# Optimization experiments

Measured on AMD Instinct MI355X. Metric: run time of the kernel, lower is better.

Reference implementation:

```python
import jax, jax.numpy as jnp
import numpy as np

CUTOFF = 8.0
N_NODES = 100000
N_EDGES = 3200000
HIDDEN = 256
VOCAB = 178


def _swish(x):
    return x * jax.nn.sigmoid(x)


def _safe_norm(v):
    # L2 norm over last axis with torch-style zero subgradient at 0
    ss = jnp.sum(v * v, axis=-1)
    return jnp.where(ss == 0, 0.0, jnp.sqrt(jnp.where(ss == 0, 1.0, ss)))


def _safe_atan2(b, a):
    # atan2 with finite grad at (0,0); forward value identical (atan2(0,0)=0)
    deg = (a == 0) & (b == 0)
    return jnp.arctan2(b, jnp.where(deg, 1.0, a))


def _scatter_argmin(d, idx, num_seg):
    # replicates torch_scatter.scatter_min argmin output (empty segments -> 0)
    E = d.shape[0]
    mn = jax.ops.segment_min(d, idx, num_segments=num_seg)
    cand = jnp.where(d == mn[idx], jnp.arange(E), E)
    am = jax.ops.segment_min(cand, idx, num_segments=num_seg)
    return jnp.where(am >= E, 0, am)


def _dist_calc(cutoff, vecs, dist, i, j, num_nodes):
    argmin0 = _scatter_argmin(dist, i, num_nodes)
    n0 = j[argmin0]
    dist1 = dist + jnp.zeros_like(dist).at[argmin0].set(cutoff)
    argmin1 = _scatter_argmin(dist1, i, num_nodes)
    n1 = j[argmin1]
    argmin0_j = _scatter_argmin(dist, j, num_nodes)
    n0_j = i[argmin0_j]
    dist1_j = dist + jnp.zeros_like(dist).at[argmin0_j].set(cutoff)
    argmin1_j = _scatter_argmin(dist1_j, j, num_nodes)
    n1_j = i[argmin1_j]

    n0 = n0[i]
    n1 = n1[i]
    n0_j = n0_j[j]
    n1_j = n1_j[j]

    idx_iref = jnp.where(n0 == j, argmin1[i], argmin0[i])
    idx_jref = jnp.where(n0_j == i, argmin1_j[j], argmin0_j[j])

    pos_ji = vecs                      # [E,3]
    pos_in0 = vecs[argmin0[i]]         # vecs[argmin0][i]
    pos_in1 = vecs[argmin1[i]]
    pos_iref = vecs[idx_iref]
    pos_jref_j = vecs[idx_jref]

    a = jnp.sum(-pos_ji * pos_in0, axis=-1)
    b = _safe_norm(jnp.cross(-pos_ji, pos_in0))
    theta = _safe_atan2(b, a)
    theta = jnp.where(theta < 0, theta + jnp.pi, theta)

    dist_ji = _safe_norm(pos_ji)

    plane1 = jnp.cross(-pos_ji, pos_in0)
    plane2 = jnp.cross(-pos_ji, pos_in1)
    a = jnp.sum(plane1 * plane2, axis=-1)
    b = jnp.sum(jnp.cross(plane1, plane2) * pos_ji, axis=-1) / dist_ji
    phi = _safe_atan2(b, a)
    phi = jnp.where(phi < 0, phi + jnp.pi, phi)

    plane1 = jnp.cross(pos_ji, pos_jref_j)
    plane2 = jnp.cross(pos_ji, pos_iref)
    a = jnp.sum(plane1 * plane2, axis=-1)
    b = jnp.sum(jnp.cross(plane1, plane2) * pos_ji, axis=-1) / dist_ji
    tau = _safe_atan2(b, a)
    tau = jnp.where(tau < 0, tau + jnp.pi, tau)

    return dist, theta, phi, tau


def setup_inputs() -> dict:
    key = jax.random.key(0)
    k1, k2, k3, k4, k5 = jax.random.split(key, 5)
    x = jax.random.randint(k1, (N_NODES,), 0, VOCAB)
    pos = jax.random.normal(k2, (N_NODES, 3), jnp.float32) * 3.0
    i = jax.random.randint(k3, (N_EDGES,), 0, N_NODES)
    off = jax.random.randint(k4, (N_EDGES,), 1, N_NODES)
    j = (i + off) % N_NODES  # no self-edges -> dist > 0
    edge_index = jnp.stack([i, j])
    emb_weight = jax.random.normal(k5, (VOCAB, HIDDEN), jnp.float32)
    return {"x": x, "pos": pos, "edge_index": edge_index, "emb_weight": emb_weight}


def reference(x, pos, edge_index, emb_weight):
    i, j = edge_index[0], edge_index[1]
    vecs = pos[j] - pos[i]          # [E,3]
    dist = _safe_norm(vecs)         # [E]
    h = _swish(emb_weight[x])       # [N,H]
    dist, theta, phi, tau = _dist_calc(CUTOFF, vecs, dist, i, j, pos.shape[0])
    return h, dist, theta, phi, tau
```

## Files before the change

kernel.cpp:

```cpp
#include <hip/hip_runtime.h>
#include <math.h>

#define HID 256
#define PI_F 3.14159265358979323846f
typedef unsigned long long ull;

struct F3 { float x, y, z; };

__device__ __forceinline__ F3 crossc(F3 a, F3 b) {
    F3 r;
    float t1 = a.z * b.y;
    r.x = __builtin_fmaf(a.y, b.z, -t1);
    float t2 = a.x * b.z;
    r.y = __builtin_fmaf(a.z, b.x, -t2);
    float t3 = a.y * b.x;
    r.z = __builtin_fmaf(a.x, b.y, -t3);
    return r;
}
__device__ __forceinline__ float dotf(F3 a, F3 b) {
#pragma clang fp contract(off)
    float px = a.x * b.x;
    float py = a.y * b.y;
    float pz = a.z * b.z;
    return (px + py) + pz;
}
__device__ __forceinline__ float sqrt_cr(float ss) {
    return (float)sqrt((double)ss);
}
__device__ __forceinline__ float safe_atan2(float b, float a) {
    float aa = (a == 0.f && b == 0.f) ? 1.f : a;
    return atan2f(b, aa);
}
__device__ __forceinline__ F3 loadp(const float* __restrict__ pos, int n) {
    F3 r;
    r.x = pos[3 * n + 0];
    r.y = pos[3 * n + 1];
    r.z = pos[3 * n + 2];
    return r;
}
__device__ __forceinline__ F3 subv(F3 a, F3 b) {
#pragma clang fp contract(off)
    F3 r;
    r.x = a.x - b.x;
    r.y = a.y - b.y;
    r.z = a.z - b.z;
    return r;
}
__device__ __forceinline__ ull umin64(ull a, ull b) { return a < b ? a : b; }

__device__ __forceinline__ unsigned xcc_id() {
    return __builtin_amdgcn_s_getreg((3u << 11) | 20u) & 7u;
}

__device__ __forceinline__ void insert2_loc(ull* __restrict__ s, unsigned db, ull key) {
    unsigned hi2 = ((const unsigned*)s)[3];
    if (db > hi2) return;
    unsigned hi1 = ((const unsigned*)s)[1];
    if (db <= hi1) {
        ull ret = __hip_atomic_fetch_min(&s[0], key, __ATOMIC_RELAXED,
                                         __HIP_MEMORY_SCOPE_WORKGROUP);
        ull loser = ret > key ? ret : key;
        if (loser != ~0ull)
            __hip_atomic_fetch_min(&s[1], loser, __ATOMIC_RELAXED,
                                   __HIP_MEMORY_SCOPE_WORKGROUP);
    } else {
        __hip_atomic_fetch_min(&s[1], key, __ATOMIC_RELAXED,
                               __HIP_MEMORY_SCOPE_WORKGROUP);
    }
}

__device__ __forceinline__ void merge8(const ull* __restrict__ slots8, size_t twoN,
                                       int n, ull& m1, ull& m2) {
    m1 = ~0ull; m2 = ~0ull;
#pragma unroll
    for (int c = 0; c < 8; c++) {
        ull a = slots8[(size_t)c * twoN + 2 * (size_t)n];
        ull b = slots8[(size_t)c * twoN + 2 * (size_t)n + 1];
        if (a < m1) { m2 = m1; m1 = a; } else if (a < m2) m2 = a;
        if (b < m1) { m2 = m1; m1 = b; } else if (b < m2) m2 = b;
    }
}

__global__ void k_pass1(const int* __restrict__ ei, const int* __restrict__ ej,
                        const float* __restrict__ pos, float* __restrict__ dist,
                        ull* __restrict__ slots8A, ull* __restrict__ slots8B,
                        const unsigned* __restrict__ thrA, const unsigned* __restrict__ thrB,
                        size_t twoN, int e0, int e1) {
#pragma clang fp contract(off)
    int e = e0 + blockIdx.x * blockDim.x + threadIdx.x;
    if (e >= e1) return;
    unsigned c = xcc_id();
    ull* sA = slots8A + (size_t)c * twoN;
    ull* sB = slots8B + (size_t)c * twoN;
    int ii = ei[e], jj = ej[e];
    F3 v = subv(loadp(pos, jj), loadp(pos, ii));
    float sx = v.x * v.x;
    float sy = v.y * v.y;
    float sz = v.z * v.z;
    float ss = (sx + sy) + sz;
    float d = (ss == 0.f) ? 0.f : sqrt_cr(ss);
    dist[e] = d;
    unsigned db = __float_as_uint(d);
    ull key = ((ull)db << 32) | (unsigned)e;
    if (db <= thrA[ii]) insert2_loc(&sA[2 * (size_t)ii], db, key);
    if (db <= thrB[jj]) insert2_loc(&sB[2 * (size_t)jj], db, key);
}

__global__ void k_snapshot(const ull* __restrict__ slots8A, const ull* __restrict__ slots8B,
                           unsigned* __restrict__ thrA, unsigned* __restrict__ thrB,
                           size_t twoN, int N) {
    int n = blockIdx.x * blockDim.x + threadIdx.x;
    if (n >= N) return;
    ull m1, m2;
    merge8(slots8A, twoN, n, m1, m2);
    thrA[n] = (unsigned)(m2 >> 32);
    merge8(slots8B, twoN, n, m1, m2);
    thrB[n] = (unsigned)(m2 >> 32);
}

__global__ void k_prep(const ull* __restrict__ slots8A, const ull* __restrict__ slots8B,
                       const int* __restrict__ ei, const int* __restrict__ ej,
                       const float* __restrict__ pos,
                       float4* __restrict__ nodeI, float4* __restrict__ nodeJ,
                       int* __restrict__ a0i, int* __restrict__ a0j,
                       unsigned* __restrict__ flags, size_t twoN, int N) {
#pragma clang fp contract(off)
    int n = blockIdx.x * blockDim.x + threadIdx.x;
    if (n >= N) return;

    ull k1, k2;
    merge8(slots8A, twoN, n, k1, k2);
    int a0, a1;
    if (k1 == ~0ull) {
        a0 = 0; a1 = 0;
        atomicOr(&flags[0], 1u);
    } else {
        a0 = (int)(k1 & 0xffffffffu);
        float d0 = __uint_as_float((unsigned)(k1 >> 32));
        ull mkey = ((ull)__float_as_uint(d0 + 8.0f) << 32) | (unsigned)a0;
        if (k2 == ~0ull) a1 = a0;
        else a1 = (mkey < k2) ? a0 : (int)(k2 & 0xffffffffu);
    }
    a0i[n] = a0;
    F3 in0 = subv(loadp(pos, ej[a0]), loadp(pos, ei[a0]));
    int n0 = ej[a0];
    F3 in1 = subv(loadp(pos, ej[a1]), loadp(pos, ei[a1]));
    nodeI[2 * (size_t)n]     = make_float4(in0.x, in0.y, in0.z, __int_as_float(n0));
    nodeI[2 * (size_t)n + 1] = make_float4(in1.x, in1.y, in1.z, 0.f);

    ull q1, q2;
    merge8(slots8B, twoN, n, q1, q2);
    int b0, b1;
    if (q1 == ~0ull) {
        b0 = 0; b1 = 0;
        atomicOr(&flags[1], 1u);
    } else {
        b0 = (int)(q1 & 0xffffffffu);
        float d0 = __uint_as_float((unsigned)(q1 >> 32));
        ull mkey = ((ull)__float_as_uint(d0 + 8.0f) << 32) | (unsigned)b0;
        if (q2 == ~0ull) b1 = b0;
        else b1 = (mkey < q2) ? b0 : (int)(q2 & 0xffffffffu);
    }
    a0j[n] = b0;
    F3 w0 = subv(loadp(pos, ej[b0]), loadp(pos, ei[b0]));
    int m0 = ei[b0];
    F3 w1 = subv(loadp(pos, ej[b1]), loadp(pos, ei[b1]));
    nodeJ[2 * (size_t)n]     = make_float4(w0.x, w0.y, w0.z, __int_as_float(m0));
    nodeJ[2 * (size_t)n + 1] = make_float4(w1.x, w1.y, w1.z, 0.f);
}

__global__ void k_fix(const unsigned* __restrict__ flags,
                      const int* __restrict__ ei, const int* __restrict__ ej,
                      const float* __restrict__ dist,
                      const int* __restrict__ a0i, const int* __restrict__ a0j,
                      const float* __restrict__ pos,
                      float4* __restrict__ nodeI, float4* __restrict__ nodeJ, int E) {
#pragma clang fp contract(off)
    __shared__ ull smin[256];
    int side = blockIdx.x;
    if (flags[side] == 0u) return;
    const int* seg = (side == 0) ? ei : ej;
    int s = seg[0];
    int marked = (side == 0) ? a0i[s] : a0j[s];
    ull local = ~0ull;
    for (int e = threadIdx.x; e < E; e += 256) {
        if (seg[e] != s) continue;
        float d = dist[e];
        float dm = (e == marked || e == 0) ? (d + 8.0f) : d;
        ull key = ((ull)__float_as_uint(dm) << 32) | (unsigned)e;
        local = umin64(local, key);
    }
    smin[threadIdx.x] = local;
    __syncthreads();
    for (int w = 128; w > 0; w >>= 1) {
        if (threadIdx.x < w) smin[threadIdx.x] = umin64(smin[threadIdx.x], smin[threadIdx.x + w]);
        __syncthreads();
    }
    if (threadIdx.x == 0) {
        int a1 = (smin[0] == ~0ull) ? 0 : (int)(smin[0] & 0xffffffffu);
        F3 v = subv(loadp(pos, ej[a1]), loadp(pos, ei[a1]));
        if (side == 0) nodeI[2 * (size_t)s + 1] = make_float4(v.x, v.y, v.z, 0.f);
        else           nodeJ[2 * (size_t)s + 1] = make_float4(v.x, v.y, v.z, 0.f);
    }
}

__global__ void k_angles(const int* __restrict__ ei, const int* __restrict__ ej,
                         const float* __restrict__ pos, const float* __restrict__ dist,
                         const float4* __restrict__ nodeI, const float4* __restrict__ nodeJ,
                         float* __restrict__ theta, float* __restrict__ phi,
                         float* __restrict__ tau, int E) {
    int e = blockIdx.x * blockDim.x + threadIdx.x;
    if (e >= E) return;
    int ii = ei[e], jj = ej[e];

    float4 A0 = nodeI[2 * (size_t)ii];
    float4 A1 = nodeI[2 * (size_t)ii + 1];
    float4 B0 = nodeJ[2 * (size_t)jj];
    float4 B1 = nodeJ[2 * (size_t)jj + 1];
    int n0 = __float_as_int(A0.w);
    int m0 = __float_as_int(B0.w);

    F3 in0; in0.x = A0.x; in0.y = A0.y; in0.z = A0.z;
    F3 in1; in1.x = A1.x; in1.y = A1.y; in1.z = A1.z;
    F3 w0;  w0.x = B0.x;  w0.y = B0.y;  w0.z = B0.z;
    F3 w1;  w1.x = B1.x;  w1.y = B1.y;  w1.z = B1.z;

    F3 iref = (n0 == jj) ? in1 : in0;
    F3 jref = (m0 == ii) ? w1 : w0;

    F3 p = subv(loadp(pos, jj), loadp(pos, ii));
    F3 mp;
    mp.x = -p.x; mp.y = -p.y; mp.z = -p.z;

    float a = dotf(mp, in0);
    F3 c1 = crossc(mp, in0);
    float ssb = dotf(c1, c1);
    float b = (ssb == 0.f) ? 0.f : sqrt_cr(ssb);
    float th = safe_atan2(b, a);
    if (th < 0.f) th += PI_F;

    float dji = dist[e];

    F3 pl2 = crossc(mp, in1);
    a = dotf(c1, pl2);
    F3 cc = crossc(c1, pl2);
    b = dotf(cc, p) / dji;
    float ph = safe_atan2(b, a);
    if (ph < 0.f) ph += PI_F;

    F3 t1 = crossc(p, jref);
    F3 t2 = crossc(p, iref);
    a = dotf(t1, t2);
    cc = crossc(t1, t2);
    b = dotf(cc, p) / dji;
    float ta = safe_atan2(b, a);
    if (ta < 0.f) ta += PI_F;

    theta[e] = th;
    phi[e] = ph;
    tau[e] = ta;
}

__global__ void k_embed(const int* __restrict__ x, const float* __restrict__ w,
                        float* __restrict__ h, int total4) {
    int t = blockIdx.x * blockDim.x + threadIdx.x;
    if (t >= total4) return;
    int n = t >> 6;
    int c = t & 63;
    int row = x[n];
    float4 v = *reinterpret_cast<const float4*>(w + (size_t)row * HID + c * 4);
    float4 o;
    o.x = v.x / (1.f + expf(-v.x));
    o.y = v.y / (1.f + expf(-v.y));
    o.z = v.z / (1.f + expf(-v.z));
    o.w = v.w / (1.f + expf(-v.w));
    *reinterpret_cast<float4*>(h + (size_t)n * HID + c * 4) = o;
}

extern "C" void kernel_launch(void* const* d_in, const int* in_sizes, int n_in,
                              void* d_out, int out_size, void* d_ws, size_t ws_size,
                              hipStream_t stream) {
    const int* x = (const int*)d_in[0];
    const float* pos = (const float*)d_in[1];
    const int* eidx = (const int*)d_in[2];
    const float* emb = (const float*)d_in[3];

    const int N = in_sizes[0];
    const int E = in_sizes[2] / 2;
    const int* ei = eidx;
    const int* ej = eidx + E;

    float* out = (float*)d_out;
    float* out_h = out;
    float* out_dist = out + (size_t)N * HID;
    float* out_theta = out_dist + E;
    float* out_phi = out_theta + E;
    float* out_tau = out_phi + E;

    size_t twoN = 2 * (size_t)N;
    ull* slots8A = (ull*)out_h;
    ull* slots8B = slots8A + 8 * twoN;
    unsigned* thrA = (unsigned*)(slots8B + 8 * twoN);
    unsigned* thrB = thrA + N;
    float4* nodeI = (float4*)(thrB + N);
    float4* nodeJ = nodeI + twoN;
    int* a0i = (int*)(nodeJ + twoN);
    int* a0j = a0i + N;
    unsigned* flags = (unsigned*)(a0j + N);

    const int BS = 256;
    int gN = (N + BS - 1) / BS;
    int total4 = N * (HID / 4);
    int gH = (total4 + BS - 1) / BS;

    hipMemsetAsync(slots8A, 0xFF, 16 * twoN * sizeof(ull) + 2 * (size_t)N * sizeof(unsigned), stream);
    hipMemsetAsync(flags, 0, 2 * sizeof(unsigned), stream);

    int bounds[5] = {0, E / 8, E / 4, E / 2, E};
    for (int k = 0; k < 4; k++) {
        int lo = bounds[k], hi = bounds[k + 1];
        if (hi <= lo) continue;
        int g = (hi - lo + BS - 1) / BS;
        k_pass1<<<g, BS, 0, stream>>>(ei, ej, pos, out_dist, slots8A, slots8B,
                                      thrA, thrB, twoN, lo, hi);
        if (k < 3)
            k_snapshot<<<gN, BS, 0, stream>>>(slots8A, slots8B, thrA, thrB, twoN, N);
    }

    k_prep<<<gN, BS, 0, stream>>>(slots8A, slots8B, ei, ej, pos,
                                  nodeI, nodeJ, a0i, a0j, flags, twoN, N);
    k_fix<<<2, BS, 0, stream>>>(flags, ei, ej, out_dist, a0i, a0j, pos,
                                nodeI, nodeJ, E);
    k_angles<<<(E + BS - 1) / BS, BS, 0, stream>>>(ei, ej, pos, out_dist, nodeI, nodeJ,
                                                   out_theta, out_phi, out_tau, E);
    k_embed<<<gH, BS, 0, stream>>>(x, emb, out_h, total4);
}
```

Before: 389.7 us.

## Drop threshold-filtered chunked pass1 and cache edge vectors for angle kernel

Replaces the four-chunk pass1 with per-node threshold snapshots by a single pass over all edges that always attempts the top-2 atomic insert. It also stores each edge's vector in a scratch buffer so the angle kernel reads 12 contiguous bytes instead of gathering two random positions. This removes three snapshot kernels and several launches. In exchange every edge now issues atomics, where before most were filtered out by the thresholds, and an extra 12-byte-per-edge write and read is added.

```diff
diff --git a/kernel.cpp b/kernel.cpp
--- a/kernel.cpp
+++ b/kernel.cpp
@@ -83,17 +83,20 @@
 
 __global__ void k_pass1(const int* __restrict__ ei, const int* __restrict__ ej,
                         const float* __restrict__ pos, float* __restrict__ dist,
+                        float* __restrict__ vecs,
                         ull* __restrict__ slots8A, ull* __restrict__ slots8B,
-                        const unsigned* __restrict__ thrA, const unsigned* __restrict__ thrB,
-                        size_t twoN, int e0, int e1) {
-#pragma clang fp contract(off)
-    int e = e0 + blockIdx.x * blockDim.x + threadIdx.x;
-    if (e >= e1) return;
+                        size_t twoN, int E) {
+#pragma clang fp contract(off)
+    int e = blockIdx.x * blockDim.x + threadIdx.x;
+    if (e >= E) return;
     unsigned c = xcc_id();
     ull* sA = slots8A + (size_t)c * twoN;
     ull* sB = slots8B + (size_t)c * twoN;
     int ii = ei[e], jj = ej[e];
     F3 v = subv(loadp(pos, jj), loadp(pos, ii));
+    vecs[3 * (size_t)e + 0] = v.x;
+    vecs[3 * (size_t)e + 1] = v.y;
+    vecs[3 * (size_t)e + 2] = v.z;
     float sx = v.x * v.x;
     float sy = v.y * v.y;
     float sz = v.z * v.z;
@@ -102,20 +105,8 @@
     dist[e] = d;
     unsigned db = __float_as_uint(d);
     ull key = ((ull)db << 32) | (unsigned)e;
-    if (db <= thrA[ii]) insert2_loc(&sA[2 * (size_t)ii], db, key);
-    if (db <= thrB[jj]) insert2_loc(&sB[2 * (size_t)jj], db, key);
-}
-
-__global__ void k_snapshot(const ull* __restrict__ slots8A, const ull* __restrict__ slots8B,
-                           unsigned* __restrict__ thrA, unsigned* __restrict__ thrB,
-                           size_t twoN, int N) {
-    int n = blockIdx.x * blockDim.x + threadIdx.x;
-    if (n >= N) return;
-    ull m1, m2;
-    merge8(slots8A, twoN, n, m1, m2);
-    thrA[n] = (unsigned)(m2 >> 32);
-    merge8(slots8B, twoN, n, m1, m2);
-    thrB[n] = (unsigned)(m2 >> 32);
+    insert2_loc(&sA[2 * (size_t)ii], db, key);
+    insert2_loc(&sB[2 * (size_t)jj], db, key);
 }
 
 __global__ void k_prep(const ull* __restrict__ slots8A, const ull* __restrict__ slots8B,
@@ -205,7 +196,7 @@
 }
 
 __global__ void k_angles(const int* __restrict__ ei, const int* __restrict__ ej,
-                         const float* __restrict__ pos, const float* __restrict__ dist,
+                         const float* __restrict__ vecs, const float* __restrict__ dist,
                          const float4* __restrict__ nodeI, const float4* __restrict__ nodeJ,
                          float* __restrict__ theta, float* __restrict__ phi,
                          float* __restrict__ tau, int E) {
@@ -228,7 +219,10 @@
     F3 iref = (n0 == jj) ? in1 : in0;
     F3 jref = (m0 == ii) ? w1 : w0;
 
-    F3 p = subv(loadp(pos, jj), loadp(pos, ii));
+    F3 p;
+    p.x = vecs[3 * (size_t)e + 0];
+    p.y = vecs[3 * (size_t)e + 1];
+    p.z = vecs[3 * (size_t)e + 2];
     F3 mp;
     mp.x = -p.x; mp.y = -p.y; mp.z = -p.z;
 
@@ -300,38 +294,29 @@
     size_t twoN = 2 * (size_t)N;
     ull* slots8A = (ull*)out_h;
     ull* slots8B = slots8A + 8 * twoN;
-    unsigned* thrA = (unsigned*)(slots8B + 8 * twoN);
-    unsigned* thrB = thrA + N;
-    float4* nodeI = (float4*)(thrB + N);
+    float4* nodeI = (float4*)(slots8B + 8 * twoN);
     float4* nodeJ = nodeI + twoN;
-    int* a0i = (int*)(nodeJ + twoN);
+    float* vecs = (float*)(nodeJ + twoN);
+    int* a0i = (int*)(vecs + 3 * (size_t)E);
     int* a0j = a0i + N;
     unsigned* flags = (unsigned*)(a0j + N);
 
     const int BS = 256;
+    int gE = (E + BS - 1) / BS;
     int gN = (N + BS - 1) / BS;
     int total4 = N * (HID / 4);
     int gH = (total4 + BS - 1) / BS;
 
-    hipMemsetAsync(slots8A, 0xFF, 16 * twoN * sizeof(ull) + 2 * (size_t)N * sizeof(unsigned), stream);
+    hipMemsetAsync(slots8A, 0xFF, 16 * twoN * sizeof(ull), stream);
     hipMemsetAsync(flags, 0, 2 * sizeof(unsigned), stream);
 
-    int bounds[5] = {0, E / 8, E / 4, E / 2, E};
-    for (int k = 0; k < 4; k++) {
-        int lo = bounds[k], hi = bounds[k + 1];
-        if (hi <= lo) continue;
-        int g = (hi - lo + BS - 1) / BS;
-        k_pass1<<<g, BS, 0, stream>>>(ei, ej, pos, out_dist, slots8A, slots8B,
-                                      thrA, thrB, twoN, lo, hi);
-        if (k < 3)
-            k_snapshot<<<gN, BS, 0, stream>>>(slots8A, slots8B, thrA, thrB, twoN, N);
-    }
-
+    k_pass1<<<gE, BS, 0, stream>>>(ei, ej, pos, out_dist, vecs,
+                                   slots8A, slots8B, twoN, E);
     k_prep<<<gN, BS, 0, stream>>>(slots8A, slots8B, ei, ej, pos,
                                   nodeI, nodeJ, a0i, a0j, flags, twoN, N);
     k_fix<<<2, BS, 0, stream>>>(flags, ei, ej, out_dist, a0i, a0j, pos,
                                 nodeI, nodeJ, E);
-    k_angles<<<(E + BS - 1) / BS, BS, 0, stream>>>(ei, ej, pos, out_dist, nodeI, nodeJ,
-                                                   out_theta, out_phi, out_tau, E);
+    k_angles<<<gE, BS, 0, stream>>>(ei, ej, vecs, out_dist, nodeI, nodeJ,
+                                    out_theta, out_phi, out_tau, E);
     k_embed<<<gH, BS, 0, stream>>>(x, emb, out_h, total4);
 }
```

Result: slower. 497.7 us (+27.7%).
